# Kernel tuning notes

Hardware: AMD Instinct MI355X
Metric: run time of the kernel (lower is better)

## Reference

```python
import jax, jax.numpy as jnp
import numpy as np

EMBED_DIM = 1024
NUM_HEADS = 16
HEAD_DIM = EMBED_DIM // NUM_HEADS
SCALING = HEAD_DIM ** -0.5


def setup_inputs() -> dict:
    key = jax.random.key(0)
    ks = jax.random.split(key, 11)
    B, S, E = 4, 2048, EMBED_DIM
    s = 1.0 / np.sqrt(E)
    return {
        "query": jax.random.normal(ks[0], (B, S, E), jnp.float32),
        "key": jax.random.normal(ks[1], (B, S, E), jnp.float32),
        "value": jax.random.normal(ks[2], (B, S, E), jnp.float32),
        "q_w": jax.random.normal(ks[3], (E, E), jnp.float32) * s,
        "q_b": jax.random.normal(ks[4], (E,), jnp.float32) * 0.01,
        "k_w": jax.random.normal(ks[5], (E, E), jnp.float32) * s,
        "k_b": jax.random.normal(ks[6], (E,), jnp.float32) * 0.01,
        "v_w": jax.random.normal(ks[7], (E, E), jnp.float32) * s,
        "v_b": jax.random.normal(ks[8], (E,), jnp.float32) * 0.01,
        "out_w": jax.random.normal(ks[9], (E, E), jnp.float32) * s,
        "out_b": jax.random.normal(ks[10], (E,), jnp.float32) * 0.01,
    }


def reference(query, key, value, q_w, q_b, k_w, k_b, v_w, v_b, out_w, out_b):
    B, S, E = query.shape
    H, D = NUM_HEADS, HEAD_DIM
    # torch Linear: x @ W.T + b
    q = (query @ q_w.T + q_b).reshape(B, S, H, D).transpose(0, 2, 1, 3)  # [B,H,S,D]
    k = (key @ k_w.T + k_b).reshape(B, -1, H, D).transpose(0, 2, 1, 3)
    v = (value @ v_w.T + v_b).reshape(B, -1, H, D).transpose(0, 2, 1, 3)
    attn_scores = jnp.einsum("bhsd,bhtd->bhst", q, k) * SCALING  # [B,H,S,S]
    attn_weights = jax.nn.softmax(attn_scores, axis=-1)
    attn_output = jnp.einsum("bhst,bhtd->bhsd", attn_weights, v)
    attn_output = attn_output.transpose(0, 2, 1, 3).reshape(B, S, E)
    return attn_output @ out_w.T + out_b
```

## Files before the change

### kernel.cpp

```cpp
#include <hip/hip_runtime.h>
#include <stdint.h>
#include <stddef.h>

#define BB 4
#define SS 2048
#define EE 1024
#define HH 16
#define DD 64
#define MTOT (BB * SS)

#define SOFTMAX_C (0.125f * 1.44269504088896340736f)

using bf16x8 = __attribute__((ext_vector_type(8))) __bf16;
using f32x4  = __attribute__((ext_vector_type(4))) float;
using s16x4  = __attribute__((ext_vector_type(4))) short;

__device__ inline unsigned short f2bf(float f) {
    union { float f; uint32_t u; } v; v.f = f;
    uint32_t u = v.u;
    u += 0x7fffu + ((u >> 16) & 1u);
    return (unsigned short)(u >> 16);
}

__device__ inline uint32_t packbf_trunc(float lo, float hi) {
    union { float f; uint32_t u; } a, b; a.f = lo; b.f = hi;
    return (a.u >> 16) | (b.u & 0xFFFF0000u);
}

__device__ inline void gld_lds16(const unsigned short* g, unsigned short* l) {
    __builtin_amdgcn_global_load_lds(
        (const __attribute__((address_space(1))) unsigned int*)g,
        (__attribute__((address_space(3))) unsigned int*)l,
        16, 0, 0);
}

__global__ __launch_bounds__(256) void cast3_f32_bf16(
    const float* __restrict__ a, const float* __restrict__ b,
    const float* __restrict__ c,
    unsigned short* __restrict__ oa, unsigned short* __restrict__ ob,
    unsigned short* __restrict__ oc, int n4) {
    int i = blockIdx.x * 256 + threadIdx.x;
    const float* src = (blockIdx.y == 0) ? a : (blockIdx.y == 1) ? b : c;
    unsigned short* dst = (blockIdx.y == 0) ? oa : (blockIdx.y == 1) ? ob : oc;
    if (i < n4) {
        float4 f = ((const float4*)src)[i];
        ushort4 o;
        o.x = f2bf(f.x); o.y = f2bf(f.y); o.z = f2bf(f.z); o.w = f2bf(f.w);
        ((ushort4*)dst)[i] = o;
    }
}

__global__ __launch_bounds__(256) void cast4_f32_bf16(
    const float* __restrict__ a, const float* __restrict__ b,
    const float* __restrict__ c, const float* __restrict__ d,
    unsigned short* __restrict__ oa, unsigned short* __restrict__ ob,
    unsigned short* __restrict__ oc, unsigned short* __restrict__ od, int n4) {
    int i = blockIdx.x * 256 + threadIdx.x;
    const float* src = (blockIdx.y == 0) ? a : (blockIdx.y == 1) ? b
                     : (blockIdx.y == 2) ? c : d;
    unsigned short* dst = (blockIdx.y == 0) ? oa : (blockIdx.y == 1) ? ob
                        : (blockIdx.y == 2) ? oc : od;
    if (i < n4) {
        float4 f = ((const float4*)src)[i];
        ushort4 o;
        o.x = f2bf(f.x); o.y = f2bf(f.y); o.z = f2bf(f.z); o.w = f2bf(f.w);
        ((ushort4*)dst)[i] = o;
    }
}

template <int MODE>
__global__ __launch_bounds__(256) void gemm_nt(
    const unsigned short* __restrict__ A,
    const unsigned short* __restrict__ W,
    const float* __restrict__ bias,
    void* __restrict__ outp, float oscale) {
    __shared__ __align__(16) unsigned short As[128 * 64];
    __shared__ __align__(16) unsigned short Bs[128 * 64];

    const int tid  = threadIdx.x;
    const int lane = tid & 63;
    const int wid  = tid >> 6;
    const int wm   = wid >> 1;
    const int wn   = wid & 1;
    const int quad = lane >> 4;
    const int l16  = lane & 15;
    const int m0   = blockIdx.y * 128;
    const int n0   = blockIdx.x * 128;

    f32x4 acc[4][4];
#pragma unroll
    for (int i = 0; i < 4; i++)
#pragma unroll
        for (int j = 0; j < 4; j++) acc[i][j] = (f32x4){0.f, 0.f, 0.f, 0.f};

    const int lrow = lane >> 3;
    const int lcol = (lane & 7) * 8;
    const unsigned short* ga = A + (size_t)(m0 + wid * 32 + lrow) * 1024 + lcol;
    const unsigned short* gb = W + (size_t)(n0 + wid * 32 + lrow) * 1024 + lcol;
    unsigned short* la = As + wid * 32 * 64;
    unsigned short* lb = Bs + wid * 32 * 64;

    for (int k0 = 0; k0 < 1024; k0 += 64) {
        __syncthreads();
#pragma unroll
        for (int c = 0; c < 4; c++) {
            gld_lds16(ga + (size_t)c * 8 * 1024 + k0, la + c * 8 * 64);
            gld_lds16(gb + (size_t)c * 8 * 1024 + k0, lb + c * 8 * 64);
        }
        __syncthreads();

#pragma unroll
        for (int kt = 0; kt < 2; kt++) {
            bf16x8 a[4], b[4];
#pragma unroll
            for (int mt = 0; mt < 4; mt++)
                a[mt] = *(const bf16x8*)(As + (wm * 64 + mt * 16 + l16) * 64 + kt * 32 + quad * 8);
#pragma unroll
            for (int nt = 0; nt < 4; nt++)
                b[nt] = *(const bf16x8*)(Bs + (wn * 64 + nt * 16 + l16) * 64 + kt * 32 + quad * 8);
#pragma unroll
            for (int mt = 0; mt < 4; mt++)
#pragma unroll
                for (int nt = 0; nt < 4; nt++)
                    acc[mt][nt] = __builtin_amdgcn_mfma_f32_16x16x32_bf16(
                        a[mt], b[nt], acc[mt][nt], 0, 0, 0);
        }
    }

#pragma unroll
    for (int mt = 0; mt < 4; mt++) {
#pragma unroll
        for (int nt = 0; nt < 4; nt++) {
            int gcol = n0 + wn * 64 + nt * 16 + l16;
            float bvn = (MODE != 3) ? bias[gcol] : 0.f;
#pragma unroll
            for (int r = 0; r < 4; r++) {
                int grow = m0 + wm * 64 + mt * 16 + quad * 4 + r;
                float bv = (MODE == 3) ? bias[grow] : bvn;
                float v = (acc[mt][nt][r] + bv) * oscale;
                if (MODE == 0) {
                    int bb = grow >> 11, sr = grow & 2047;
                    int hh = gcol >> 6,  dd = gcol & 63;
                    ((unsigned short*)outp)[(((size_t)(bb * HH + hh)) * SS + sr) * DD + dd] = f2bf(v);
                } else if (MODE == 3) {
                    int bb = gcol >> 11, sr = gcol & 2047;
                    int hh = grow >> 6,  dd = grow & 63;
                    ((unsigned short*)outp)[(((size_t)(bb * HH + hh)) * DD + dd) * SS + sr] = f2bf(v);
                } else {
                    ((float*)outp)[(size_t)grow * 1024 + gcol] = v;
                }
            }
        }
    }
}

__global__ __launch_bounds__(256) void flash_attn5(
    const unsigned short* __restrict__ Qh,
    const unsigned short* __restrict__ Kh,
    const unsigned short* __restrict__ Vtg,
    unsigned short* __restrict__ attn) {
    constexpr int LS = 72;
    __shared__ __align__(16) unsigned short Sh[128 * LS];
    unsigned short* Ks = Sh;
    unsigned short* Vs = Sh + 64 * LS;

    const int tid  = threadIdx.x;
    const int lane = tid & 63;
    const int w    = tid >> 6;
    const int quad = lane >> 4;
    const int l16  = lane & 15;
    const int bh   = blockIdx.y;
    const int q0   = blockIdx.x * 128;
    const size_t base = (size_t)bh * SS * DD;

    union { unsigned short u[4]; s16x4 v; } onesu;
#pragma unroll
    for (int i = 0; i < 4; i++) onesu.u[i] = 0x3F80;
    const s16x4 ones = onesu.v;

    bf16x8 bq[2][2];
#pragma unroll
    for (int s = 0; s < 2; s++)
#pragma unroll
        for (int kt = 0; kt < 2; kt++)
            bq[s][kt] = *(const bf16x8*)(Qh + base +
                (size_t)(q0 + w * 32 + s * 16 + l16) * DD + kt * 32 + quad * 8);

    f32x4 oT[2][4];
    f32x4 lacc[2];
#pragma unroll
    for (int s = 0; s < 2; s++) {
        lacc[s] = (f32x4){0.f, 0.f, 0.f, 0.f};
#pragma unroll
        for (int dt = 0; dt < 4; dt++) oT[s][dt] = (f32x4){0.f, 0.f, 0.f, 0.f};
    }

    for (int j0 = 0; j0 < SS; j0 += 64) {
        __syncthreads();
#pragma unroll
        for (int i = 0; i < 2; i++) {
            int c = tid + 256 * i;
            int row = c >> 3, col8 = (c & 7) * 8;
            *(uint4*)(Ks + row * LS + col8) =
                *(const uint4*)(Kh + base + (size_t)(j0 + row) * DD + col8);
            *(uint4*)(Vs + row * LS + col8) =
                *(const uint4*)(Vtg + base + (size_t)row * SS + j0 + col8);
        }
        __syncthreads();

        f32x4 sacc[2][4];
#pragma unroll
        for (int s = 0; s < 2; s++)
#pragma unroll
            for (int mt = 0; mt < 4; mt++) sacc[s][mt] = (f32x4){0.f, 0.f, 0.f, 0.f};
#pragma unroll
        for (int kt = 0; kt < 2; kt++) {
            bf16x8 ak[4];
#pragma unroll
            for (int mt = 0; mt < 4; mt++)
                ak[mt] = *(const bf16x8*)(Ks + (mt * 16 + l16) * LS + kt * 32 + quad * 8);
#pragma unroll
            for (int s = 0; s < 2; s++)
#pragma unroll
                for (int mt = 0; mt < 4; mt++)
                    sacc[s][mt] = __builtin_amdgcn_mfma_f32_16x16x32_bf16(
                        ak[mt], bq[s][kt], sacc[s][mt], 0, 0, 0);
        }

        s16x4 bpf[2][4];
#pragma unroll
        for (int s = 0; s < 2; s++) {
#pragma unroll
            for (int mt = 0; mt < 4; mt++) {
                float p0 = __builtin_amdgcn_exp2f(sacc[s][mt][0]);
                float p1 = __builtin_amdgcn_exp2f(sacc[s][mt][1]);
                float p2 = __builtin_amdgcn_exp2f(sacc[s][mt][2]);
                float p3 = __builtin_amdgcn_exp2f(sacc[s][mt][3]);
                union { uint32_t w[2]; s16x4 v; } pk;
                pk.w[0] = packbf_trunc(p0, p1);
                pk.w[1] = packbf_trunc(p2, p3);
                bpf[s][mt] = pk.v;
                lacc[s] = __builtin_amdgcn_mfma_f32_16x16x16bf16_1k(
                    ones, pk.v, lacc[s], 0, 0, 0);
            }
        }

#pragma unroll
        for (int mt = 0; mt < 4; mt++) {
#pragma unroll
            for (int dt = 0; dt < 4; dt++) {
                s16x4 av = *(const s16x4*)(Vs + (dt * 16 + l16) * LS + mt * 16 + quad * 4);
#pragma unroll
                for (int s = 0; s < 2; s++)
                    oT[s][dt] = __builtin_amdgcn_mfma_f32_16x16x16bf16_1k(
                        av, bpf[s][mt], oT[s][dt], 0, 0, 0);
            }
        }
    }

    float inv_l[2];
#pragma unroll
    for (int s = 0; s < 2; s++) inv_l[s] = 1.f / lacc[s][0];

    __syncthreads();
#pragma unroll
    for (int s = 0; s < 2; s++)
#pragma unroll
        for (int dt = 0; dt < 4; dt++)
#pragma unroll
            for (int r = 0; r < 4; r++)
                Sh[(w * 32 + s * 16 + l16) * LS + dt * 16 + quad * 4 + r] =
                    f2bf(oT[s][dt][r] * inv_l[s]);
    __syncthreads();

    const int b = bh >> 4, h = bh & 15;
#pragma unroll
    for (int i = 0; i < 4; i++) {
        int c = tid + 256 * i;
        int row = c >> 3, col8 = (c & 7) * 8;
        *(uint4*)(attn + ((size_t)b * SS + q0 + row) * EE + h * 64 + col8) =
            *(const uint4*)(Sh + row * LS + col8);
    }
}

extern "C" void kernel_launch(void* const* d_in, const int* in_sizes, int n_in,
                              void* d_out, int out_size, void* d_ws, size_t ws_size,
                              hipStream_t stream) {
    (void)in_sizes; (void)n_in; (void)out_size; (void)ws_size;
    const float* q_in  = (const float*)d_in[0];
    const float* k_in  = (const float*)d_in[1];
    const float* v_in  = (const float*)d_in[2];
    const float* q_w   = (const float*)d_in[3];
    const float* q_b   = (const float*)d_in[4];
    const float* k_w   = (const float*)d_in[5];
    const float* k_b   = (const float*)d_in[6];
    const float* v_w   = (const float*)d_in[7];
    const float* v_b   = (const float*)d_in[8];
    const float* out_w = (const float*)d_in[9];
    const float* out_b = (const float*)d_in[10];

    const size_t NX = (size_t)MTOT * EE;
    const size_t NW = (size_t)EE * EE;

    unsigned short* xq = (unsigned short*)d_ws;
    unsigned short* xk = xq + NX;
    unsigned short* xv = xk + NX;
    unsigned short* wq = xv + NX;
    unsigned short* wk = wq + NW;
    unsigned short* wv = wk + NW;
    unsigned short* wo = wv + NW;
    unsigned short* qh = wo + NW;
    unsigned short* kh = qh + NX;
    unsigned short* vt = kh + NX;
    unsigned short* attn = vt + NX;

    cast3_f32_bf16<<<dim3((int)(NX / 4 / 256), 3), 256, 0, stream>>>(
        q_in, k_in, v_in, xq, xk, xv, (int)(NX / 4));
    cast4_f32_bf16<<<dim3((int)(NW / 4 / 256), 4), 256, 0, stream>>>(
        q_w, k_w, v_w, out_w, wq, wk, wv, wo, (int)(NW / 4));

    dim3 ggrid(EE / 128, MTOT / 128);
    dim3 ggridT(MTOT / 128, EE / 128);
    gemm_nt<0><<<ggrid, 256, 0, stream>>>(xq, wq, q_b, qh, SOFTMAX_C);
    gemm_nt<0><<<ggrid, 256, 0, stream>>>(xk, wk, k_b, kh, 1.0f);
    gemm_nt<3><<<ggridT, 256, 0, stream>>>(wv, xv, v_b, vt, 1.0f);

    flash_attn5<<<dim3(SS / 128, BB * HH), 256, 0, stream>>>(qh, kh, vt, attn);

    gemm_nt<1><<<ggrid, 256, 0, stream>>>(attn, wo, out_b, (float*)d_out, 1.0f);
}
```

Before: 412.1 us.

## Double-buffer K/V tiles in flash attention with register prefetch and MFMA priority

The flash attention kernel now prefetches the next K/V tile from global memory into registers while computing on the current LDS buffer, then stores it into a second LDS buffer. This leaves one barrier per iteration instead of two and hides global load latency behind the MFMA work. It also pads the V stride to 76 to reduce LDS bank conflicts and raises wave priority around the MFMA sections. In exchange it doubles LDS use and adds registers for the prefetch, which may lower occupancy.

```diff
diff --git a/kernel.cpp b/kernel.cpp
--- a/kernel.cpp
+++ b/kernel.cpp
@@ -154,15 +154,16 @@
     }
 }
 
-__global__ __launch_bounds__(256) void flash_attn5(
+__global__ __launch_bounds__(256) void flash_attn6(
     const unsigned short* __restrict__ Qh,
     const unsigned short* __restrict__ Kh,
     const unsigned short* __restrict__ Vtg,
     unsigned short* __restrict__ attn) {
-    constexpr int LS = 72;
-    __shared__ __align__(16) unsigned short Sh[128 * LS];
-    unsigned short* Ks = Sh;
-    unsigned short* Vs = Sh + 64 * LS;
+    constexpr int LSK = 72;
+    constexpr int LSV = 76;
+    constexpr int BUFSZ = 64 * LSK + 64 * LSV;
+    constexpr int NT = SS / 64;
+    __shared__ __align__(16) unsigned short Sh[2 * BUFSZ];
 
     const int tid  = threadIdx.x;
     const int lane = tid & 63;
@@ -195,30 +196,40 @@
         for (int dt = 0; dt < 4; dt++) oT[s][dt] = (f32x4){0.f, 0.f, 0.f, 0.f};
     }
 
-    for (int j0 = 0; j0 < SS; j0 += 64) {
-        __syncthreads();
-#pragma unroll
-        for (int i = 0; i < 2; i++) {
-            int c = tid + 256 * i;
-            int row = c >> 3, col8 = (c & 7) * 8;
-            *(uint4*)(Ks + row * LS + col8) =
-                *(const uint4*)(Kh + base + (size_t)(j0 + row) * DD + col8);
-            *(uint4*)(Vs + row * LS + col8) =
-                *(const uint4*)(Vtg + base + (size_t)row * SS + j0 + col8);
-        }
-        __syncthreads();
-
+    const int crow = tid >> 3;
+    const int ccol = (tid & 7) * 8;
+    uint4 kreg[2], vreg[2];
+
+    auto LOADT = [&](int j0) {
+#pragma unroll
+        for (int i = 0; i < 2; ++i) {
+            kreg[i] = *(const uint4*)(Kh + base + (size_t)(j0 + crow + 32 * i) * DD + ccol);
+            vreg[i] = *(const uint4*)(Vtg + base + (size_t)(crow + 32 * i) * SS + j0 + ccol);
+        }
+    };
+    auto STORET = [&](unsigned short* KsD, unsigned short* VsD) {
+#pragma unroll
+        for (int i = 0; i < 2; ++i) {
+            int row = crow + 32 * i;
+            *(uint4*)(KsD + row * LSK + ccol) = kreg[i];
+            *(uint2*)(VsD + row * LSV + ccol)     = uint2{vreg[i].x, vreg[i].y};
+            *(uint2*)(VsD + row * LSV + ccol + 4) = uint2{vreg[i].z, vreg[i].w};
+        }
+    };
+
+    auto COMPUTE = [&](const unsigned short* Ks, const unsigned short* Vs) {
         f32x4 sacc[2][4];
 #pragma unroll
         for (int s = 0; s < 2; s++)
 #pragma unroll
             for (int mt = 0; mt < 4; mt++) sacc[s][mt] = (f32x4){0.f, 0.f, 0.f, 0.f};
+        __builtin_amdgcn_s_setprio(1);
 #pragma unroll
         for (int kt = 0; kt < 2; kt++) {
             bf16x8 ak[4];
 #pragma unroll
             for (int mt = 0; mt < 4; mt++)
-                ak[mt] = *(const bf16x8*)(Ks + (mt * 16 + l16) * LS + kt * 32 + quad * 8);
+                ak[mt] = *(const bf16x8*)(Ks + (mt * 16 + l16) * LSK + kt * 32 + quad * 8);
 #pragma unroll
             for (int s = 0; s < 2; s++)
 #pragma unroll
@@ -226,6 +237,7 @@
                     sacc[s][mt] = __builtin_amdgcn_mfma_f32_16x16x32_bf16(
                         ak[mt], bq[s][kt], sacc[s][mt], 0, 0, 0);
         }
+        __builtin_amdgcn_s_setprio(0);
 
         s16x4 bpf[2][4];
 #pragma unroll
@@ -245,17 +257,37 @@
             }
         }
 
+        __builtin_amdgcn_s_setprio(1);
 #pragma unroll
         for (int mt = 0; mt < 4; mt++) {
 #pragma unroll
             for (int dt = 0; dt < 4; dt++) {
-                s16x4 av = *(const s16x4*)(Vs + (dt * 16 + l16) * LS + mt * 16 + quad * 4);
+                s16x4 av = *(const s16x4*)(Vs + (dt * 16 + l16) * LSV + mt * 16 + quad * 4);
 #pragma unroll
                 for (int s = 0; s < 2; s++)
                     oT[s][dt] = __builtin_amdgcn_mfma_f32_16x16x16bf16_1k(
                         av, bpf[s][mt], oT[s][dt], 0, 0, 0);
             }
         }
+        __builtin_amdgcn_s_setprio(0);
+    };
+
+    LOADT(0);
+    STORET(Sh, Sh + 64 * LSK);
+    __syncthreads();
+
+    for (int jt = 0; jt < NT - 1; ++jt) {
+        const int cur = jt & 1;
+        const unsigned short* Ks = Sh + cur * BUFSZ;
+        LOADT((jt + 1) * 64);
+        COMPUTE(Ks, Ks + 64 * LSK);
+        unsigned short* Kn = Sh + (cur ^ 1) * BUFSZ;
+        STORET(Kn, Kn + 64 * LSK);
+        __syncthreads();
+    }
+    {
+        const unsigned short* Ks = Sh + ((NT - 1) & 1) * BUFSZ;
+        COMPUTE(Ks, Ks + 64 * LSK);
     }
 
     float inv_l[2];
@@ -269,7 +301,7 @@
         for (int dt = 0; dt < 4; dt++)
 #pragma unroll
             for (int r = 0; r < 4; r++)
-                Sh[(w * 32 + s * 16 + l16) * LS + dt * 16 + quad * 4 + r] =
+                Sh[(w * 32 + s * 16 + l16) * LSK + dt * 16 + quad * 4 + r] =
                     f2bf(oT[s][dt][r] * inv_l[s]);
     __syncthreads();
 
@@ -279,7 +311,7 @@
         int c = tid + 256 * i;
         int row = c >> 3, col8 = (c & 7) * 8;
         *(uint4*)(attn + ((size_t)b * SS + q0 + row) * EE + h * 64 + col8) =
-            *(const uint4*)(Sh + row * LS + col8);
+            *(const uint4*)(Sh + row * LSK + col8);
     }
 }
 
@@ -325,7 +357,7 @@
     gemm_nt<0><<<ggrid, 256, 0, stream>>>(xk, wk, k_b, kh, 1.0f);
     gemm_nt<3><<<ggridT, 256, 0, stream>>>(wv, xv, v_b, vt, 1.0f);
 
-    flash_attn5<<<dim3(SS / 128, BB * HH), 256, 0, stream>>>(qh, kh, vt, attn);
+    flash_attn6<<<dim3(SS / 128, BB * HH), 256, 0, stream>>>(qh, kh, vt, attn);
 
     gemm_nt<1><<<ggrid, 256, 0, stream>>>(attn, wo, out_b, (float*)d_out, 1.0f);
 }
```

Result: faster. 396.6 us (-3.8%).
